# Kernel optimization log

Hardware: AMD Instinct MI355X
Metric: run time of the kernel (lower is better)

Reference implementation:

```python
import jax, jax.numpy as jnp
import numpy as np


def setup_inputs() -> dict:
    key = jax.random.key(0)
    k1, k2 = jax.random.split(key)
    B, C, H, W, P = 8, 128, 512, 512, 2048
    imgs = jax.random.normal(k1, (B, C, H, W), dtype=jnp.float32)
    batch_points = jax.random.randint(k2, (B, P, 2), 0, 512, dtype=jnp.int64)
    return {"imgs": imgs, "batch_points": batch_points}


def reference(imgs, batch_points):
    # imgs: [B, C, H, W]; batch_points: [B, P, 2] with (x, y) per point.
    # Original loops: for each image, for each point, take img[:, y, x] (a C-vector),
    # then cat + reshape to [total_points, C]. Vectorized as one batched gather.
    B, C, H, W = imgs.shape
    pts = batch_points.astype(jnp.int32)
    x = pts[..., 0]  # [B, P]
    y = pts[..., 1]  # [B, P]
    b = jnp.arange(B)[:, None]  # [B, 1]
    crops = imgs[b, :, y, x]  # [B, P, C] (image-major, point order matches the loop)
    out = crops.reshape(B * pts.shape[1], C)
    length = out.shape[0]
    return out, length
```

## Files before the change

kernel.cpp:

```cpp
#include <hip/hip_runtime.h>

#define NB 8
#define NC 128
#define NH 512
#define NW 512
#define NP 2048

__global__ __launch_bounds__(256) void crop_gather_kernel(
    const float* __restrict__ imgs,
    const int* __restrict__ pts,
    float* __restrict__ out)
{
    int tid = blockIdx.x * 256 + threadIdx.x;
    int row = tid >> 5;
    int t   = tid & 31;
    int c0  = t << 2;

    int x = pts[row * 2 + 0];
    int y = pts[row * 2 + 1];
    int b = row >> 11;

    const size_t plane = (size_t)NH * NW;
    const float* src = imgs + ((size_t)(b * NC + c0)) * plane
                            + (size_t)y * NW + (size_t)x;

    float4 v;
    v.x = src[0];
    v.y = src[plane];
    v.z = src[2 * plane];
    v.w = src[3 * plane];

    *reinterpret_cast<float4*>(out + (size_t)row * NC + c0) = v;

    if (tid == 0) {
        out[(size_t)NB * NP * NC] = 16384.0f;
    }
}

extern "C" void kernel_launch(void* const* d_in, const int* in_sizes, int n_in,
                              void* d_out, int out_size, void* d_ws, size_t ws_size,
                              hipStream_t stream) {
    const float* imgs = (const float*)d_in[0];
    const int* pts = (const int*)d_in[1];
    float* out = (float*)d_out;

    const int total_threads = NB * NP * NC / 4;
    const int block = 256;
    const int grid = total_threads / block;

    crop_gather_kernel<<<grid, block, 0, stream>>>(imgs, pts, out);
}
```

Before: 46.72 us.

## Bucket-sort points by row before gathering to improve cache locality

Adds a per-image counting sort of points by y coordinate into a workspace permutation, packing x, y and the original index into one word. The gather kernel then walks the points in sorted order and writes each result back to its original output row. The aim is to make nearby warps touch the same image rows for better L2 and TLB reuse. It costs an extra kernel launch and scattered output rows, and falls back to the old kernel when the workspace is too small.

After: 49.62 us. +6.2%, slower.

```diff
diff --git a/kernel.cpp b/kernel.cpp
--- a/kernel.cpp
+++ b/kernel.cpp
@@ -6,6 +6,82 @@
 #define NW 512
 #define NP 2048
 
+__global__ __launch_bounds__(512) void sort_points_kernel(
+    const int* __restrict__ pts, unsigned* __restrict__ perm)
+{
+    int b = blockIdx.x;
+    __shared__ unsigned hist[512];
+    __shared__ unsigned scan_buf[512];
+
+    int t = threadIdx.x;
+    hist[t] = 0;
+    __syncthreads();
+
+    unsigned recs[4];
+    int base = b * NP;
+    #pragma unroll
+    for (int i = 0; i < 4; ++i) {
+        int p = t + i * 512;
+        unsigned x = (unsigned)pts[(base + p) * 2 + 0];
+        unsigned y = (unsigned)pts[(base + p) * 2 + 1];
+        recs[i] = (y << 20) | (x << 11) | (unsigned)p;
+        atomicAdd(&hist[y], 1u);
+    }
+    __syncthreads();
+
+    unsigned own = hist[t];
+    scan_buf[t] = own;
+    __syncthreads();
+    for (int d = 1; d < 512; d <<= 1) {
+        unsigned add = (t >= d) ? scan_buf[t - d] : 0u;
+        __syncthreads();
+        scan_buf[t] += add;
+        __syncthreads();
+    }
+    hist[t] = scan_buf[t] - own;
+    __syncthreads();
+
+    #pragma unroll
+    for (int i = 0; i < 4; ++i) {
+        unsigned y = recs[i] >> 20;
+        unsigned pos = atomicAdd(&hist[y], 1u);
+        perm[b * NP + pos] = recs[i];
+    }
+}
+
+__global__ __launch_bounds__(256) void crop_gather_sorted_kernel(
+    const float* __restrict__ imgs,
+    const unsigned* __restrict__ perm,
+    float* __restrict__ out)
+{
+    int tid = blockIdx.x * 256 + threadIdx.x;
+    int srow = tid >> 5;
+    int lane = tid & 31;
+    int c0 = lane << 2;
+
+    unsigned rec = perm[srow];
+    int p = (int)(rec & 0x7FFu);
+    int x = (int)((rec >> 11) & 0x1FFu);
+    int y = (int)(rec >> 20);
+    int b = srow >> 11;
+
+    const size_t plane = (size_t)NH * NW;
+    const float* src = imgs + ((size_t)(b * NC + c0)) * plane
+                            + (size_t)y * NW + (size_t)x;
+    float4 v;
+    v.x = src[0];
+    v.y = src[plane];
+    v.z = src[2 * plane];
+    v.w = src[3 * plane];
+
+    size_t orow = (size_t)(b * NP + p);
+    *reinterpret_cast<float4*>(out + orow * NC + c0) = v;
+
+    if (tid == 0) {
+        out[(size_t)NB * NP * NC] = 16384.0f;
+    }
+}
+
 __global__ __launch_bounds__(256) void crop_gather_kernel(
     const float* __restrict__ imgs,
     const int* __restrict__ pts,
@@ -13,8 +89,8 @@
 {
     int tid = blockIdx.x * 256 + threadIdx.x;
     int row = tid >> 5;
-    int t   = tid & 31;
-    int c0  = t << 2;
+    int t = tid & 31;
+    int c0 = t << 2;
 
     int x = pts[row * 2 + 0];
     int y = pts[row * 2 + 1];
@@ -23,13 +99,11 @@
     const size_t plane = (size_t)NH * NW;
     const float* src = imgs + ((size_t)(b * NC + c0)) * plane
                             + (size_t)y * NW + (size_t)x;
-
     float4 v;
     v.x = src[0];
     v.y = src[plane];
     v.z = src[2 * plane];
     v.w = src[3 * plane];
-
     *reinterpret_cast<float4*>(out + (size_t)row * NC + c0) = v;
 
     if (tid == 0) {
@@ -45,8 +119,13 @@
     float* out = (float*)d_out;
 
     const int total_threads = NB * NP * NC / 4;
-    const int block = 256;
-    const int grid = total_threads / block;
+    const int grid = total_threads / 256;
 
-    crop_gather_kernel<<<grid, block, 0, stream>>>(imgs, pts, out);
+    if (ws_size >= (size_t)NB * NP * sizeof(unsigned)) {
+        unsigned* perm = (unsigned*)d_ws;
+        sort_points_kernel<<<NB, 512, 0, stream>>>(pts, perm);
+        crop_gather_sorted_kernel<<<grid, 256, 0, stream>>>(imgs, perm, out);
+    } else {
+        crop_gather_kernel<<<grid, 256, 0, stream>>>(imgs, pts, out);
+    }
 }
```
